# Kernel tuning notes

Measured on AMD Instinct MI355X. Metric: run time of the kernel, lower is better.

The kernel has to match this reference:

```python
import jax, jax.numpy as jnp
import numpy as np

N = 50000      # nodes per type
E = 200000     # edges per relation
H, D = 4, 64   # heads, per-head dim
C = H * D      # hidden = hc_graph * heads = 256
L = 3          # num_hops (HGTConv layers)
HC_LIN, HC_TASK = 256, 128
OUT_DIMS = (3, 3, 3, 5, 1, 1, 8)  # ptr_l1/l2/l3, leaf_category, signed, floating, size


def setup_inputs() -> dict:
    key = jax.random.key(0)
    ks = jax.random.split(key, 24)
    f = lambda k, s: jax.random.normal(k, s, dtype=jnp.float32) * 0.05
    ri = lambda k: jax.random.randint(k, (E,), 0, N, dtype=jnp.int32)
    return {
        "xe": f(ks[0], (N, C)),
        "xs": f(ks[1], (N, C)),
        "ee_src": ri(ks[2]), "ee_dst": ri(ks[3]),
        "es_src": ri(ks[4]), "es_dst": ri(ks[5]),
        "se_src": ri(ks[6]), "se_dst": ri(ks[7]),
        # per-layer, per-node-type projections (2 node types)
        "Wk": f(ks[8], (L, 2, C, C)),
        "Wq": f(ks[9], (L, 2, C, C)),
        "Wv": f(ks[10], (L, 2, C, C)),
        "Wa": f(ks[11], (L, 2, C, C)),
        "skip": jnp.ones((L, 2), dtype=jnp.float32),
        # per-layer, per-relation attention/message transforms (3 relations)
        "Arel": f(ks[12], (L, 3, H, D, D)),
        "Mrel": f(ks[13], (L, 3, H, D, D)),
        "mu": jnp.ones((L, 3, H), dtype=jnp.float32),
        # shared linear stack + 7 task heads (final out padded to 8, sliced per head)
        "Wsh": f(ks[14], (2, HC_LIN, HC_LIN)),
        "bsh": jnp.zeros((2, HC_LIN), dtype=jnp.float32),
        "Wt1": f(ks[15], (7, HC_LIN, HC_TASK)),
        "bt1": jnp.zeros((7, HC_TASK), dtype=jnp.float32),
        "Wt2": f(ks[16], (7, HC_TASK, 8)),
        "bt2": jnp.zeros((7, 8), dtype=jnp.float32),
    }


def _seg_softmax(scores, seg, n):
    m = jax.ops.segment_max(scores, seg, num_segments=n)
    e = jnp.exp(scores - m[seg])
    s = jax.ops.segment_sum(e, seg, num_segments=n)
    return e / (s[seg] + 1e-16)


def _hgt_forward(xe, xs, ee_src, ee_dst, es_src, es_dst, se_src, se_dst,
                 Wk, Wq, Wv, Wa, skip, Arel, Mrel, mu, Wsh, bsh, Wt1, bt1, Wt2, bt2):
    inv_sqrt_d = 1.0 / jnp.sqrt(jnp.float32(D))

    def rel(k_src, v_src, q_dst, src, dst, A, M, m):
        kt = jnp.einsum('ehd,hdf->ehf', k_src[src], A)          # [E,H,D]
        score = (q_dst[dst] * kt).sum(-1) * (m * inv_sqrt_d)    # [E,H]
        msg = jnp.einsum('ehd,hdf->ehf', v_src[src], M)         # [E,H,D]
        return score, msg

    for l in range(L):
        ke = (xe @ Wk[l, 0]).reshape(N, H, D)
        qe = (xe @ Wq[l, 0]).reshape(N, H, D)
        ve = (xe @ Wv[l, 0]).reshape(N, H, D)
        ks_ = (xs @ Wk[l, 1]).reshape(N, H, D)
        qs = (xs @ Wq[l, 1]).reshape(N, H, D)
        vs = (xs @ Wv[l, 1]).reshape(N, H, D)

        s0, m0 = rel(ke, ve, qe, ee_src, ee_dst, Arel[l, 0], Mrel[l, 0], mu[l, 0])  # expr->expr
        s1, m1 = rel(ke, ve, qs, es_src, es_dst, Arel[l, 1], Mrel[l, 1], mu[l, 1])  # expr->stmt
        s2, m2 = rel(ks_, vs, qe, se_src, se_dst, Arel[l, 2], Mrel[l, 2], mu[l, 2])  # stmt->expr

        # destination 'expr': softmax over all incoming edges (rel0 + rel2)
        sc_e = jnp.concatenate([s0, s2], axis=0)
        ms_e = jnp.concatenate([m0, m2], axis=0)
        dst_e = jnp.concatenate([ee_dst, se_dst], axis=0)
        a_e = _seg_softmax(sc_e, dst_e, N)
        agg_e = jax.ops.segment_sum(a_e[..., None] * ms_e, dst_e, num_segments=N).reshape(N, C)

        # destination 'stmt': only rel1
        a_s = _seg_softmax(s1, es_dst, N)
        agg_s = jax.ops.segment_sum(a_s[..., None] * m1, es_dst, num_segments=N).reshape(N, C)

        be = jax.nn.sigmoid(skip[l, 0])
        bs = jax.nn.sigmoid(skip[l, 1])
        xe = be * (jax.nn.gelu(agg_e, approximate=False) @ Wa[l, 0]) + (1.0 - be) * xe
        xs = bs * (jax.nn.gelu(agg_s, approximate=False) @ Wa[l, 1]) + (1.0 - bs) * xs

    # shared linear stack on 'expr' nodes
    h = xe
    for i in range(Wsh.shape[0]):
        h = jax.nn.relu(h @ Wsh[i] + bsh[i])

    # 7 task heads: hidden layer + final (padded to 8 outputs, sliced per head)
    t = jax.nn.relu(jnp.einsum('nc,kct->knt', h, Wt1) + bt1[:, None, :])  # [7,N,HC_TASK]
    o = jnp.einsum('knt,kto->kno', t, Wt2) + bt2[:, None, :]              # [7,N,8]
    outs = [o[i, :, :d] for i, d in enumerate(OUT_DIMS)]
    return jnp.concatenate(outs, axis=-1)  # [N, 24]


def reference(xe, xs, ee_src, ee_dst, es_src, es_dst, se_src, se_dst,
              Wk, Wq, Wv, Wa, skip, Arel, Mrel, mu, Wsh, bsh, Wt1, bt1, Wt2, bt2):
    return _hgt_forward(xe, xs, ee_src, ee_dst, es_src, es_dst, se_src, se_dst,
                        Wk, Wq, Wv, Wa, skip, Arel, Mrel, mu, Wsh, bsh, Wt1, bt1, Wt2, bt2)
```

## Files before the change

kernel.cpp:

```cpp
#include <hip/hip_runtime.h>
#include <hip/hip_fp16.h>
#include <cmath>


#define CDIM 256
#define AR_R (256 * 256)

using f16x8 = __attribute__((ext_vector_type(8))) _Float16;
using f16x4 = __attribute__((ext_vector_type(4))) _Float16;
using f16x2 = __attribute__((ext_vector_type(2))) _Float16;
using f32x4 = __attribute__((ext_vector_type(4))) float;

__device__ __forceinline__ float gelu_f(float x) {
    return 0.5f * x * (1.0f + erff(x * 0.70710678118654752f));
}

__device__ __forceinline__ float dot8f(const f16x8 a, const f16x8 b, float r) {
#if __has_builtin(__builtin_amdgcn_fdot2)
#pragma unroll
    for (int t = 0; t < 4; ++t) {
        f16x2 av = {a[2 * t], a[2 * t + 1]};
        f16x2 bv = {b[2 * t], b[2 * t + 1]};
        r = __builtin_amdgcn_fdot2(av, bv, r, false);
    }
#else
#pragma unroll
    for (int t = 0; t < 8; ++t) r += (float)a[t] * (float)b[t];
#endif
    return r;
}

__global__ __launch_bounds__(256) void zero_k(int* __restrict__ p, size_t n) {
    size_t i = (size_t)blockIdx.x * blockDim.x + threadIdx.x;
    const size_t stride = (size_t)gridDim.x * blockDim.x;
    for (; i < n; i += stride) p[i] = 0;
}

__global__ __launch_bounds__(256) void cvt_k(const float* __restrict__ in,
                                             _Float16* __restrict__ out,
                                             size_t n4) {
    size_t i = (size_t)blockIdx.x * blockDim.x + threadIdx.x;
    const size_t stride = (size_t)gridDim.x * blockDim.x;
    for (; i < n4; i += stride) {
        const float4 v = ((const float4*)in)[i];
        f16x4 o;
        o[0] = (_Float16)v.x; o[1] = (_Float16)v.y;
        o[2] = (_Float16)v.z; o[3] = (_Float16)v.w;
        ((f16x4*)out)[i] = o;
    }
}

__device__ __forceinline__ void cvtT_dev(const float* __restrict__ W,
                                         _Float16* __restrict__ dst) {
    const int o = blockIdx.x, c = threadIdx.x;
    dst[(size_t)o * 256 + c] = (_Float16)W[(size_t)c * 256 + o];
}

__device__ __forceinline__ void foldT_dev(const float* __restrict__ Wbase,
                                          const float* __restrict__ T,
                                          _Float16* __restrict__ dst) {
    __shared__ float row[256];
    const int c = blockIdx.x, t = threadIdx.x;
    row[t] = Wbase[(size_t)c * 256 + t];
    __syncthreads();
    const int h = t >> 6, f = t & 63;
    const float* Th = T + h * 4096;
    float acc = 0.f;
#pragma unroll 8
    for (int d = 0; d < 64; ++d) acc += row[h * 64 + d] * Th[d * 64 + f];
    dst[(size_t)t * 256 + c] = (_Float16)acc;
}

__global__ __launch_bounds__(256) void prep_layer_k(
    const float* __restrict__ Wk, const float* __restrict__ Wq,
    const float* __restrict__ Wv, const float* __restrict__ Wa,
    const float* __restrict__ Arel, const float* __restrict__ Mrel, int l,
    _Float16* __restrict__ arena) {
    const size_t CC = 65536, HDD = 16384;
    _Float16* L = arena + (size_t)l * 10 * AR_R;
    const float* Wk0 = Wk + (l * 2 + 0) * CC;
    const float* Wk1 = Wk + (l * 2 + 1) * CC;
    const float* Wv0 = Wv + (l * 2 + 0) * CC;
    const float* Wv1 = Wv + (l * 2 + 1) * CC;
    switch (blockIdx.y) {
        case 0: cvtT_dev(Wq + (l * 2 + 0) * CC, L); break;
        case 1: foldT_dev(Wk0, Arel + (l * 3 + 0) * HDD, L + 1 * AR_R); break;
        case 2: foldT_dev(Wk0, Arel + (l * 3 + 1) * HDD, L + 2 * AR_R); break;
        case 3: cvtT_dev(Wq + (l * 2 + 1) * CC, L + 3 * AR_R); break;
        case 4: foldT_dev(Wk1, Arel + (l * 3 + 2) * HDD, L + 4 * AR_R); break;
        case 5: foldT_dev(Wv0, Mrel + (l * 3 + 0) * HDD, L + 5 * AR_R); break;
        case 6: foldT_dev(Wv0, Mrel + (l * 3 + 1) * HDD, L + 6 * AR_R); break;
        case 7: foldT_dev(Wv1, Mrel + (l * 3 + 2) * HDD, L + 7 * AR_R); break;
        case 8: cvtT_dev(Wa + (l * 2 + 0) * CC, L + 8 * AR_R); break;
        case 9: cvtT_dev(Wa + (l * 2 + 1) * CC, L + 9 * AR_R); break;
    }
}

__global__ __launch_bounds__(256) void prep_stack_k(const float* __restrict__ Wsh,
                                                    _Float16* __restrict__ SA) {
    cvtT_dev(Wsh + (size_t)blockIdx.y * 65536, SA + (size_t)blockIdx.y * AR_R);
}

__global__ __launch_bounds__(256) void prep_heads_k(const float* __restrict__ Wt1,
                                                    _Float16* __restrict__ HA) {
    const int o = blockIdx.x, k = blockIdx.y, c = threadIdx.x;
    HA[(size_t)(k * 128 + o) * 256 + c] =
        (_Float16)Wt1[(size_t)k * 256 * 128 + (size_t)c * 128 + o];
}

template <int EPI, bool SPLIT>
__device__ __forceinline__ void gemm_body(
    const _Float16* __restrict__ A, const _Float16* __restrict__ Bt,
    _Float16* __restrict__ C, int M, int Nc, int bm, int bn, size_t bufStride,
    const float* __restrict__ bias, const float* __restrict__ skipv,
    _Float16* As, _Float16* Bs) {
    const int tid = threadIdx.x;
    const int wave = tid >> 6, lane = tid & 63;
    const int wm = (wave >> 1) * 64, wn = (wave & 1) * 64;
    const int l15 = lane & 15, g = lane >> 4;
    const int srow = tid >> 3;
    const int sbyte = (tid & 7) * 16;

    f32x4 acc[4][4] = {};

    for (int k0 = 0; k0 < 256; k0 += 64) {
        __syncthreads();
#pragma unroll
        for (int p = 0; p < 4; ++p) {
            const int r = p * 32 + srow;
            int gr = bm + r; if (gr >= M) gr = M - 1;
            const f16x8 av = *(const f16x8*)((const char*)A +
                                             ((size_t)gr * 256 + k0) * 2 + sbyte);
            const f16x8 bv = *(const f16x8*)((const char*)Bt +
                                             ((size_t)(bn + r) * 256 + k0) * 2 + sbyte);
            const int wb = sbyte ^ ((r & 7) << 4);
            *(f16x8*)((char*)As + r * 128 + wb) = av;
            *(f16x8*)((char*)Bs + r * 128 + wb) = bv;
        }
        __syncthreads();
#pragma unroll
        for (int sub = 0; sub < 2; ++sub) {
            f16x8 af[4], bf[4];
#pragma unroll
            for (int i = 0; i < 4; ++i) {
                const int ra = wm + i * 16 + l15;
                const int rb = wn + i * 16 + l15;
                const int ka = (sub * 64 + g * 16) ^ ((ra & 7) << 4);
                const int kb = (sub * 64 + g * 16) ^ ((rb & 7) << 4);
                af[i] = *(const f16x8*)((const char*)As + ra * 128 + ka);
                bf[i] = *(const f16x8*)((const char*)Bs + rb * 128 + kb);
            }
#pragma unroll
            for (int mi = 0; mi < 4; ++mi)
#pragma unroll
                for (int ni = 0; ni < 4; ++ni)
                    acc[mi][ni] = __builtin_amdgcn_mfma_f32_16x16x32_f16(
                        af[mi], bf[ni], acc[mi][ni], 0, 0, 0);
        }
    }

    float be = 0.f, ombe = 0.f;
    if (EPI == 1) {
        const float s = skipv[0];
        be = 1.0f / (1.0f + expf(-s));
        ombe = 1.0f - be;
    }
#pragma unroll
    for (int mi = 0; mi < 4; ++mi) {
#pragma unroll
        for (int r = 0; r < 4; ++r) {
            const int row = bm + wm + mi * 16 + g * 4 + r;
            if (row >= M) continue;
#pragma unroll
            for (int ni = 0; ni < 4; ++ni) {
                const int colg = bn + wn + ni * 16 + l15;
                float v = acc[mi][ni][r];
                size_t idx;
                if (SPLIT)
                    idx = (size_t)(colg >> 8) * bufStride + (size_t)row * 256 +
                          (colg & 255);
                else
                    idx = (size_t)row * Nc + colg;
                if (EPI == 1) v = be * v + ombe * (float)C[idx];
                if (EPI == 2) v = fmaxf(v + bias[colg], 0.f);
                C[idx] = (_Float16)v;
            }
        }
    }
}

template <int EPI, bool SPLIT>
__global__ __launch_bounds__(256) void gemm_h(
    const _Float16* __restrict__ A, const _Float16* __restrict__ Bt,
    _Float16* __restrict__ C, int M, int Nc, size_t bufStride,
    const float* __restrict__ bias, const float* __restrict__ skipv) {
    __shared__ _Float16 As[128 * 64];
    __shared__ _Float16 Bs[128 * 64];
    gemm_body<EPI, SPLIT>(A, Bt, C, M, Nc, blockIdx.y * 128, blockIdx.x * 128,
                          bufStride, bias, skipv, As, Bs);
}

__global__ __launch_bounds__(256) void update2_k(
    const _Float16* __restrict__ aggE, const _Float16* __restrict__ aggS,
    const _Float16* __restrict__ WaT0, const _Float16* __restrict__ WaT1,
    _Float16* __restrict__ xeH, _Float16* __restrict__ xsH,
    const float* __restrict__ skipb, int M) {
    __shared__ _Float16 As[128 * 64];
    __shared__ _Float16 Bs[128 * 64];
    const int sel = blockIdx.x >> 1;
    const int bn = (blockIdx.x & 1) * 128;
    const int bm = blockIdx.y * 128;
    if (sel == 0)
        gemm_body<1, false>(aggE, WaT0, xeH, M, 256, bm, bn, 0, nullptr, skipb,
                            As, Bs);
    else
        gemm_body<1, false>(aggS, WaT1, xsH, M, 256, bm, bn, 0, nullptr,
                            skipb + 1, As, Bs);
}

__global__ __launch_bounds__(256) void hist3_k(const int* __restrict__ d0,
                                               const int* __restrict__ d1,
                                               const int* __restrict__ d2,
                                               int* __restrict__ cnt, int N,
                                               int E) {
    const int i = blockIdx.x * 256 + threadIdx.x;
    if (i >= E) return;
    const int r = blockIdx.y;
    const int* d = r == 0 ? d0 : r == 1 ? d1 : d2;
    atomicAdd(&cnt[(size_t)r * N + d[i]], 1);
}

__global__ __launch_bounds__(1024) void scan3_k(const int* __restrict__ cnt,
                                                int* __restrict__ rp, int N) {
    __shared__ int sums[1024];
    const int r = blockIdx.y;
    const int* c = cnt + (size_t)r * N;
    int* o = rp + (size_t)r * (N + 1);
    const int tid = threadIdx.x;
    const int chunk = (N + 1023) / 1024;
    const int lo = min(tid * chunk, N), hi = min(lo + chunk, N);
    int s = 0;
    for (int i = lo; i < hi; ++i) s += c[i];
    sums[tid] = s;
    __syncthreads();
    for (int off = 1; off < 1024; off <<= 1) {
        const int v = (tid >= off) ? sums[tid - off] : 0;
        __syncthreads();
        sums[tid] += v;
        __syncthreads();
    }
    int run = (tid == 0) ? 0 : sums[tid - 1];
    for (int i = lo; i < hi; ++i) { o[i] = run; run += c[i]; }
    if (tid == 1023) o[N] = run;
}

__global__ __launch_bounds__(256) void scatter3_k(
    const int* __restrict__ d0, const int* __restrict__ d1,
    const int* __restrict__ d2, const int* __restrict__ s0_,
    const int* __restrict__ s1_, const int* __restrict__ s2_,
    const int* __restrict__ rp, int* __restrict__ fill,
    int* __restrict__ colsrc, int N, int E) {
    const int i = blockIdx.x * 256 + threadIdx.x;
    if (i >= E) return;
    const int r = blockIdx.y;
    const int* d = r == 0 ? d0 : r == 1 ? d1 : d2;
    const int* s = r == 0 ? s0_ : r == 1 ? s1_ : s2_;
    const int dd = d[i];
    const int p = rp[(size_t)r * (N + 1) + dd] + atomicAdd(&fill[(size_t)r * N + dd], 1);
    colsrc[(size_t)r * E + p] = s[i];
}

__device__ __forceinline__ void score_rel_g(
    const f16x8 q0, const f16x8 q1, const _Float16* __restrict__ kA,
    const int* __restrict__ cs, int beg, int end, float scl,
    float* __restrict__ sc, int grp, int j, float& m) {
    for (int i = beg + grp; i < end; i += 4) {
        const int s = cs[i];
        const _Float16* row = &kA[(size_t)s * 256 + j * 16];
        const f16x8 k0 = *(const f16x8*)row;
        const f16x8 k1 = *(const f16x8*)(row + 8);
        float p = dot8f(q1, k1, dot8f(q0, k0, 0.f));
        p += __shfl_xor(p, 1);
        p += __shfl_xor(p, 2);
        const float v = p * scl;
        if ((j & 3) == 0) {
            sc[(size_t)i * 4 + (j >> 2)] = v;
            m = fmaxf(m, v);
        }
    }
}

__global__ __launch_bounds__(256) void score3_k(
    const _Float16* __restrict__ qe, const _Float16* __restrict__ kA0,
    const _Float16* __restrict__ kA1, const _Float16* __restrict__ qs,
    const _Float16* __restrict__ kA2, const int* __restrict__ rp,
    const int* __restrict__ colsrc, const float* __restrict__ muL,
    float* __restrict__ sc, float* __restrict__ mx_e,
    float* __restrict__ mx_s, int N, int E) {
    const int wid = (blockIdx.x * blockDim.x + threadIdx.x) >> 6;
    if (wid >= N) return;
    const int lane = threadIdx.x & 63;
    const int grp = lane >> 4, j = lane & 15, h = j >> 2;
    const size_t E4 = (size_t)E * 4;
    float m = -1e30f;
    if (blockIdx.y == 0) {
        const _Float16* qrow = &qe[(size_t)wid * 256 + j * 16];
        const f16x8 q0 = *(const f16x8*)qrow;
        const f16x8 q1 = *(const f16x8*)(qrow + 8);
        score_rel_g(q0, q1, kA0, colsrc, rp[wid], rp[wid + 1],
                    muL[0 * 4 + h] * 0.125f, sc, grp, j, m);
        const int* rp2 = rp + 2 * (N + 1);
        score_rel_g(q0, q1, kA2, colsrc + 2 * (size_t)E, rp2[wid], rp2[wid + 1],
                    muL[2 * 4 + h] * 0.125f, sc + 2 * E4, grp, j, m);
        m = fmaxf(m, __shfl_xor(m, 16));
        m = fmaxf(m, __shfl_xor(m, 32));
        if (grp == 0 && (j & 3) == 0) mx_e[(size_t)wid * 4 + h] = m;
    } else {
        const _Float16* qrow = &qs[(size_t)wid * 256 + j * 16];
        const f16x8 q0 = *(const f16x8*)qrow;
        const f16x8 q1 = *(const f16x8*)(qrow + 8);
        const int* rp1 = rp + (N + 1);
        score_rel_g(q0, q1, kA1, colsrc + (size_t)E, rp1[wid], rp1[wid + 1],
                    muL[1 * 4 + h] * 0.125f, sc + E4, grp, j, m);
        m = fmaxf(m, __shfl_xor(m, 16));
        m = fmaxf(m, __shfl_xor(m, 32));
        if (grp == 0 && (j & 3) == 0) mx_s[(size_t)wid * 4 + h] = m;
    }
}

__device__ __forceinline__ void agg_rel_on(
    const float* __restrict__ sc, const _Float16* __restrict__ vM,
    const int* __restrict__ cs, int beg, int end, float mh, int grp, int j,
    int h, float* accf, float& den) {
    for (int i = beg + grp; i < end; i += 4) {
        const int s = cs[i];
        const float w = expf(sc[(size_t)i * 4 + h] - mh);
        den += w;
        const _Float16* row = &vM[(size_t)s * 256 + j * 16];
        const f16x8 v0 = *(const f16x8*)row;
        const f16x8 v1 = *(const f16x8*)(row + 8);
#pragma unroll
        for (int t = 0; t < 8; ++t) accf[t] += w * (float)v0[t];
#pragma unroll
        for (int t = 0; t < 8; ++t) accf[8 + t] += w * (float)v1[t];
    }
}

__global__ __launch_bounds__(256) void agg3_k(
    const float* __restrict__ sc, const _Float16* __restrict__ vM0,
    const _Float16* __restrict__ vM1, const _Float16* __restrict__ vM2,
    const int* __restrict__ rp, const int* __restrict__ colsrc,
    const float* __restrict__ mx_e, const float* __restrict__ mx_s,
    _Float16* __restrict__ outE, _Float16* __restrict__ outS, int N, int E) {
    const int wid = (blockIdx.x * blockDim.x + threadIdx.x) >> 6;
    if (wid >= N) return;
    const int lane = threadIdx.x & 63;
    const int grp = lane >> 4, j = lane & 15, h = j >> 2;
    const size_t E4 = (size_t)E * 4;
    float accf[16] = {};
    float den = 0.f;
    _Float16* outp;
    if (blockIdx.y == 0) {
        const float mh = mx_e[(size_t)wid * 4 + h];
        const int b0 = rp[wid], e0 = rp[wid + 1];
        const int* rp2 = rp + 2 * (N + 1);
        const int b2 = rp2[wid], e2 = rp2[wid + 1];
        agg_rel_on(sc, vM0, colsrc, b0, e0, mh, grp, j, h, accf, den);
        agg_rel_on(sc + 2 * E4, vM2, colsrc + 2 * (size_t)E, b2, e2, mh, grp,
                   j, h, accf, den);
        outp = outE;
    } else {
        const float mh = mx_s[(size_t)wid * 4 + h];
        const int* rp1 = rp + (N + 1);
        const int b1 = rp1[wid], e1 = rp1[wid + 1];
        agg_rel_on(sc + E4, vM1, colsrc + (size_t)E, b1, e1, mh, grp, j, h,
                   accf, den);
        outp = outS;
    }
    den += __shfl_xor(den, 16);
    den += __shfl_xor(den, 32);
#pragma unroll
    for (int t = 0; t < 16; ++t) {
        accf[t] += __shfl_xor(accf[t], 16);
        accf[t] += __shfl_xor(accf[t], 32);
    }
    const float dinv = 1.0f / (den + 1e-16f);
    f16x4 o;
#pragma unroll
    for (int t = 0; t < 4; ++t)
        o[t] = (_Float16)gelu_f(accf[grp * 4 + t] * dinv);
    *(f16x4*)&outp[(size_t)wid * 256 + j * 16 + grp * 4] = o;
}

__global__ __launch_bounds__(256) void head2_k(const _Float16* __restrict__ t,
                                               const float* __restrict__ Wt2,
                                               const float* __restrict__ bt2,
                                               float* __restrict__ out, int M) {
    const int k = blockIdx.y;
    __shared__ float Ws[128 * 8];
    __shared__ float bs[8];
    const int tid = threadIdx.x;
    const float* W2 = Wt2 + (size_t)k * 1024;
    for (int i = tid; i < 1024; i += 256) Ws[i] = W2[i];
    if (tid < 8) bs[tid] = bt2[k * 8 + tid];
    __syncthreads();
    const int OFFA[7] = {0, 3, 6, 9, 14, 15, 16};
    const int DIMSA[7] = {3, 3, 3, 5, 1, 1, 8};
    const int nl = tid >> 3, o = tid & 7;
    const int n = blockIdx.x * 32 + nl;
    if (n >= M) return;
    const _Float16* tr = &t[(size_t)n * 896 + k * 128];
    float acc = bs[o];
#pragma unroll 8
    for (int d = 0; d < 128; ++d) acc += (float)tr[d] * Ws[d * 8 + o];
    if (o < DIMSA[k]) out[(size_t)n * 24 + OFFA[k] + o] = acc;
}


extern "C" void kernel_launch(void* const* d_in, const int* in_sizes, int n_in,
                              void* d_out, int out_size, void* d_ws,
                              size_t ws_size, hipStream_t stream) {
    const float* xe_in = (const float*)d_in[0];
    const float* xs_in = (const float*)d_in[1];
    const int* ee_src = (const int*)d_in[2];
    const int* ee_dst = (const int*)d_in[3];
    const int* es_src = (const int*)d_in[4];
    const int* es_dst = (const int*)d_in[5];
    const int* se_src = (const int*)d_in[6];
    const int* se_dst = (const int*)d_in[7];
    const float* Wk = (const float*)d_in[8];
    const float* Wq = (const float*)d_in[9];
    const float* Wv = (const float*)d_in[10];
    const float* Wa = (const float*)d_in[11];
    const float* skip = (const float*)d_in[12];
    const float* Arel = (const float*)d_in[13];
    const float* Mrel = (const float*)d_in[14];
    const float* mu = (const float*)d_in[15];
    const float* Wsh = (const float*)d_in[16];
    const float* bsh = (const float*)d_in[17];
    const float* Wt1 = (const float*)d_in[18];
    const float* bt1 = (const float*)d_in[19];
    const float* Wt2 = (const float*)d_in[20];
    const float* bt2 = (const float*)d_in[21];
    float* out = (float*)d_out;

    const int N = in_sizes[0] / CDIM;
    const int E = in_sizes[2];
    const size_t NC = (size_t)N * CDIM;
    const size_t E4 = (size_t)E * 4;
    const size_t N4 = (size_t)N * 4;

    const size_t halfs = 7 * NC + 32 * (size_t)AR_R + 7 * 32768;
    const size_t floats = 3 * E4 + 2 * N4;
    const size_t ints = 3 * (size_t)(N + 1) + 3 * (size_t)E + 3 * (size_t)N;
    const size_t need = halfs * 2 + floats * 4 + ints * 4;
    if (ws_size < need) return;

    _Float16* xeH = (_Float16*)d_ws;
    _Float16* xsH = xeH + NC;
    _Float16* Hb = xsH + NC;
    _Float16* H1 = Hb;
    _Float16* H2 = Hb + NC;
    _Float16* H3 = Hb + 2 * NC;
    _Float16* H4 = Hb + 3 * NC;
    _Float16* H5 = Hb + 4 * NC;
    _Float16* arena = Hb + 5 * NC;
    _Float16* SA = arena + (size_t)30 * AR_R;
    _Float16* HA = SA + (size_t)2 * AR_R;
    float* sc = (float*)(HA + (size_t)7 * 32768);
    float* mx_e = sc + 3 * E4;
    float* mx_s = mx_e + N4;
    int* rp = (int*)(mx_s + N4);
    int* colsrc = rp + 3 * (size_t)(N + 1);
    int* cnt = colsrc + 3 * (size_t)E;

    const int gx = (N + 127) / 128;
    const dim3 e3((E + 255) / 256, 3);
    const int wave_blocks = (N + 3) / 4;
    const int zc_blocks = (3 * N + 255) / 256;

    zero_k<<<zc_blocks, 256, 0, stream>>>(cnt, 3 * (size_t)N);
    hist3_k<<<e3, 256, 0, stream>>>(ee_dst, es_dst, se_dst, cnt, N, E);
    scan3_k<<<dim3(1, 3), 1024, 0, stream>>>(cnt, rp, N);
    zero_k<<<zc_blocks, 256, 0, stream>>>(cnt, 3 * (size_t)N);
    scatter3_k<<<e3, 256, 0, stream>>>(ee_dst, es_dst, se_dst, ee_src, es_src,
                                       se_src, rp, cnt, colsrc, N, E);

    for (int l = 0; l < 3; ++l)
        prep_layer_k<<<dim3(256, 10), 256, 0, stream>>>(Wk, Wq, Wv, Wa, Arel,
                                                        Mrel, l, arena);
    prep_stack_k<<<dim3(256, 2), 256, 0, stream>>>(Wsh, SA);
    prep_heads_k<<<dim3(128, 7), 256, 0, stream>>>(Wt1, HA);

    cvt_k<<<1024, 256, 0, stream>>>(xe_in, xeH, NC / 4);
    cvt_k<<<1024, 256, 0, stream>>>(xs_in, xsH, NC / 4);

    for (int l = 0; l < 3; ++l) {
        _Float16* L = arena + (size_t)l * 10 * AR_R;
        gemm_h<0, true><<<dim3(6, gx), 256, 0, stream>>>(
            xeH, L, H1, N, 768, NC, nullptr, nullptr);
        gemm_h<0, true><<<dim3(4, gx), 256, 0, stream>>>(
            xsH, L + 3 * AR_R, H4, N, 512, NC, nullptr, nullptr);
        score3_k<<<dim3(wave_blocks, 2), 256, 0, stream>>>(
            H1, H2, H3, H4, H5, rp, colsrc, mu + l * 12, sc, mx_e, mx_s, N, E);
        gemm_h<0, true><<<dim3(4, gx), 256, 0, stream>>>(
            xeH, L + 5 * AR_R, H2, N, 512, NC, nullptr, nullptr);
        gemm_h<0, false><<<dim3(2, gx), 256, 0, stream>>>(
            xsH, L + 7 * AR_R, H5, N, 256, 0, nullptr, nullptr);
        agg3_k<<<dim3(wave_blocks, 2), 256, 0, stream>>>(
            sc, H2, H3, H5, rp, colsrc, mx_e, mx_s, H1, H4, N, E);
        update2_k<<<dim3(4, gx), 256, 0, stream>>>(
            H1, H4, L + 8 * AR_R, L + 9 * AR_R, xeH, xsH, skip + l * 2, N);
    }

    gemm_h<2, false><<<dim3(2, gx), 256, 0, stream>>>(xeH, SA, H5, N, 256, 0,
                                                      bsh, nullptr);
    gemm_h<2, false><<<dim3(2, gx), 256, 0, stream>>>(H5, SA + AR_R, xsH, N,
                                                      256, 0, bsh + 256, nullptr);
    gemm_h<2, false><<<dim3(7, gx), 256, 0, stream>>>(xsH, HA, Hb, N, 896, 0,
                                                      bt1, nullptr);
    head2_k<<<dim3((N + 31) / 32, 7), 256, 0, stream>>>(Hb, Wt2, bt2, out, N);
}
```

Baseline: 1.167 ms.

## Use direct global-to-LDS loads in GEMM and parallelize CSR row-pointer scan

GEMM tile staging now uses global_load_lds to copy 16-byte chunks straight into LDS. The XOR swizzle moves to the global source address, so the LDS layout stays compatible with the existing fragment reads, and the register round trip is avoided. The single-block-per-relation CSR scan with serial per-thread chunks is replaced by a three-kernel scan: block partials, a scan of the partials, then a per-block write. This exposes much more parallelism at the cost of two extra launches. PB must be at most 256 (N ≤ 65536), and the 16-byte global_load_lds width requires hardware support.

```diff
diff --git a/kernel.cpp b/kernel.cpp
--- a/kernel.cpp
+++ b/kernel.cpp
@@ -118,8 +118,6 @@
     const int wave = tid >> 6, lane = tid & 63;
     const int wm = (wave >> 1) * 64, wn = (wave & 1) * 64;
     const int l15 = lane & 15, g = lane >> 4;
-    const int srow = tid >> 3;
-    const int sbyte = (tid & 7) * 16;
 
     f32x4 acc[4][4] = {};
 
@@ -127,15 +125,20 @@
         __syncthreads();
 #pragma unroll
         for (int p = 0; p < 4; ++p) {
-            const int r = p * 32 + srow;
+            const int slot = p * 256 + tid;
+            const int r = slot >> 3;
+            const int cb = ((slot & 7) << 4) ^ ((r & 7) << 4);
             int gr = bm + r; if (gr >= M) gr = M - 1;
-            const f16x8 av = *(const f16x8*)((const char*)A +
-                                             ((size_t)gr * 256 + k0) * 2 + sbyte);
-            const f16x8 bv = *(const f16x8*)((const char*)Bt +
-                                             ((size_t)(bn + r) * 256 + k0) * 2 + sbyte);
-            const int wb = sbyte ^ ((r & 7) << 4);
-            *(f16x8*)((char*)As + r * 128 + wb) = av;
-            *(f16x8*)((char*)Bs + r * 128 + wb) = bv;
+            __builtin_amdgcn_global_load_lds(
+                (const __attribute__((address_space(1))) void*)
+                    ((const char*)A + ((size_t)gr * 256 + k0) * 2 + cb),
+                (__attribute__((address_space(3))) void*)((char*)As + slot * 16),
+                16, 0, 0);
+            __builtin_amdgcn_global_load_lds(
+                (const __attribute__((address_space(1))) void*)
+                    ((const char*)Bt + ((size_t)(bn + r) * 256 + k0) * 2 + cb),
+                (__attribute__((address_space(3))) void*)((char*)Bs + slot * 16),
+                16, 0, 0);
         }
         __syncthreads();
 #pragma unroll
@@ -230,28 +233,59 @@
     atomicAdd(&cnt[(size_t)r * N + d[i]], 1);
 }
 
-__global__ __launch_bounds__(1024) void scan3_k(const int* __restrict__ cnt,
-                                                int* __restrict__ rp, int N) {
-    __shared__ int sums[1024];
-    const int r = blockIdx.y;
-    const int* c = cnt + (size_t)r * N;
-    int* o = rp + (size_t)r * (N + 1);
-    const int tid = threadIdx.x;
-    const int chunk = (N + 1023) / 1024;
-    const int lo = min(tid * chunk, N), hi = min(lo + chunk, N);
-    int s = 0;
-    for (int i = lo; i < hi; ++i) s += c[i];
-    sums[tid] = s;
+__global__ __launch_bounds__(256) void partial_k(const int* __restrict__ cnt,
+                                                 int* __restrict__ partials,
+                                                 int N, int PB) {
+    const int r = blockIdx.y, b = blockIdx.x, tid = threadIdx.x;
+    const int gi = b * 256 + tid;
+    int v = (gi < N) ? cnt[(size_t)r * N + gi] : 0;
+#pragma unroll
+    for (int o = 1; o < 64; o <<= 1) v += __shfl_xor(v, o);
+    __shared__ int ws[4];
+    if ((tid & 63) == 0) ws[tid >> 6] = v;
     __syncthreads();
-    for (int off = 1; off < 1024; off <<= 1) {
-        const int v = (tid >= off) ? sums[tid - off] : 0;
+    if (tid == 0) partials[r * PB + b] = ws[0] + ws[1] + ws[2] + ws[3];
+}
+
+__global__ __launch_bounds__(256) void scanp_k(int* __restrict__ partials,
+                                               int* __restrict__ rp, int N,
+                                               int PB, int E) {
+    __shared__ int lds[256];
+    const int r = blockIdx.y, tid = threadIdx.x;
+    const int v = (tid < PB) ? partials[r * PB + tid] : 0;
+    lds[tid] = v;
+    __syncthreads();
+    int acc = v;
+    for (int off = 1; off < 256; off <<= 1) {
+        const int t = (tid >= off) ? lds[tid - off] : 0;
         __syncthreads();
-        sums[tid] += v;
+        acc += t;
+        lds[tid] = acc;
         __syncthreads();
     }
-    int run = (tid == 0) ? 0 : sums[tid - 1];
-    for (int i = lo; i < hi; ++i) { o[i] = run; run += c[i]; }
-    if (tid == 1023) o[N] = run;
+    if (tid < PB) partials[r * PB + tid] = acc - v;
+    if (tid == 0) rp[(size_t)r * (N + 1) + N] = E;
+}
+
+__global__ __launch_bounds__(256) void rpwrite_k(const int* __restrict__ cnt,
+                                                 const int* __restrict__ partials,
+                                                 int* __restrict__ rp, int N,
+                                                 int PB) {
+    __shared__ int lds[256];
+    const int r = blockIdx.y, b = blockIdx.x, tid = threadIdx.x;
+    const int gi = b * 256 + tid;
+    const int v = (gi < N) ? cnt[(size_t)r * N + gi] : 0;
+    lds[tid] = v;
+    __syncthreads();
+    int acc = v;
+    for (int off = 1; off < 256; off <<= 1) {
+        const int t = (tid >= off) ? lds[tid - off] : 0;
+        __syncthreads();
+        acc += t;
+        lds[tid] = acc;
+        __syncthreads();
+    }
+    if (gi < N) rp[(size_t)r * (N + 1) + gi] = partials[r * PB + b] + acc - v;
 }
 
 __global__ __launch_bounds__(256) void scatter3_k(
@@ -449,10 +483,12 @@
     const size_t NC = (size_t)N * CDIM;
     const size_t E4 = (size_t)E * 4;
     const size_t N4 = (size_t)N * 4;
+    const int PB = (N + 255) / 256;
 
     const size_t halfs = 7 * NC + 32 * (size_t)AR_R + 7 * 32768;
     const size_t floats = 3 * E4 + 2 * N4;
-    const size_t ints = 3 * (size_t)(N + 1) + 3 * (size_t)E + 3 * (size_t)N;
+    const size_t ints =
+        3 * (size_t)(N + 1) + 3 * (size_t)E + 3 * (size_t)N + 3 * (size_t)PB;
     const size_t need = halfs * 2 + floats * 4 + ints * 4;
     if (ws_size < need) return;
 
@@ -473,15 +509,19 @@
     int* rp = (int*)(mx_s + N4);
     int* colsrc = rp + 3 * (size_t)(N + 1);
     int* cnt = colsrc + 3 * (size_t)E;
+    int* partials = cnt + 3 * (size_t)N;
 
     const int gx = (N + 127) / 128;
     const dim3 e3((E + 255) / 256, 3);
+    const dim3 p3(PB, 3);
     const int wave_blocks = (N + 3) / 4;
     const int zc_blocks = (3 * N + 255) / 256;
 
     zero_k<<<zc_blocks, 256, 0, stream>>>(cnt, 3 * (size_t)N);
     hist3_k<<<e3, 256, 0, stream>>>(ee_dst, es_dst, se_dst, cnt, N, E);
-    scan3_k<<<dim3(1, 3), 1024, 0, stream>>>(cnt, rp, N);
+    partial_k<<<p3, 256, 0, stream>>>(cnt, partials, N, PB);
+    scanp_k<<<dim3(1, 3), 256, 0, stream>>>(partials, rp, N, PB, E);
+    rpwrite_k<<<p3, 256, 0, stream>>>(cnt, partials, rp, N, PB);
     zero_k<<<zc_blocks, 256, 0, stream>>>(cnt, 3 * (size_t)N);
     scatter3_k<<<e3, 256, 0, stream>>>(ee_dst, es_dst, se_dst, ee_src, es_src,
                                        se_src, rp, cnt, colsrc, N, E);
```

New measurement: 1.098 ms. 1.06x faster.
